# Kernel optimization log

Measured on AMD Instinct MI355X. Metric: run time of the kernel, lower is better.

## Reference

```python
import jax, jax.numpy as jnp
import numpy as np

N = 100_000        # nodes
E = 3_200_000      # edges (avg degree 32)
F_IN = 256         # feature_num
HID = 32           # hard-coded hidden dim in TwoLayerModel
F_OUT = 64         # output_num


def setup_inputs() -> dict:
    key = jax.random.key(0)
    k0, k1, k2, k3 = jax.random.split(key, 4)
    x = jax.random.normal(k0, (N, F_IN), dtype=jnp.float32)
    edge_index = jax.random.randint(k1, (2, E), 0, N, dtype=jnp.int32)
    # glorot-ish init for the two linear weights, zero bias (matches reset_parameters)
    W1 = jax.random.normal(k2, (F_IN, HID), dtype=jnp.float32) * np.float32(1.0 / np.sqrt(F_IN))
    b1 = jnp.zeros((HID,), dtype=jnp.float32)
    W2 = jax.random.normal(k3, (HID, F_OUT), dtype=jnp.float32) * np.float32(1.0 / np.sqrt(HID))
    b2 = jnp.zeros((F_OUT,), dtype=jnp.float32)
    return {"x": x, "edge_index": edge_index, "W1": W1, "b1": b1, "W2": W2, "b2": b2}


def _gcn_propagate(h, row, col, n):
    """Symmetric-normalized sum aggregation: out[i] = sum_{(j->i)} d_j^-1/2 d_i^-1/2 h[j].
    Matches PyG gcn_norm / NewSampleModelLayer edge_weight (deg computed on col)."""
    deg = jax.ops.segment_sum(jnp.ones_like(col, dtype=h.dtype), col, num_segments=n)
    dinv = jnp.where(deg > 0, deg ** -0.5, 0.0)
    norm = dinv[row] * dinv[col]                      # [E']
    return jax.ops.segment_sum(norm[:, None] * h[row], col, num_segments=n)


def reference(x, edge_index, W1, b1, W2, b2):
    n = x.shape[0]
    sl = jnp.arange(n, dtype=edge_index.dtype)
    row = jnp.concatenate([edge_index[0], sl])        # add self-loops
    col = jnp.concatenate([edge_index[1], sl])
    # layer 1: GCNConv(feature_num, 32) -> relu (dropout inactive in eval)
    h = _gcn_propagate(x @ W1, row, col, n) + b1
    h = jax.nn.relu(h)
    # layer 2 (NewSampleModelLayer, eval path): propagate then linear projection
    fr = _gcn_propagate(h, row, col, n)
    return fr @ W2 + b2
```

## Files before the change

kernel.cpp:

```cpp
#include <hip/hip_runtime.h>
#include <hip/hip_fp16.h>
#include <math.h>


#define SHIFT1 8
#define S1 256
#define MAXNB1 400

typedef _Float16 half8 __attribute__((ext_vector_type(8)));
typedef float f32x4 __attribute__((ext_vector_type(4)));

__global__ void k_zero(int* p, int n) {
    int i = blockIdx.x * blockDim.x + threadIdx.x;
    if (i < n) p[i] = 0;
}

__global__ void k_hist1(const int4* __restrict__ cols4, int* __restrict__ bcnt,
                        int e4, int etail, const int* __restrict__ cols, int nb) {
    __shared__ int h[MAXNB1];
    for (int i = threadIdx.x; i < nb; i += blockDim.x) h[i] = 0;
    __syncthreads();
    for (int i = blockIdx.x * blockDim.x + threadIdx.x; i < e4; i += gridDim.x * blockDim.x) {
        int4 c = cols4[i];
        atomicAdd(&h[c.x >> SHIFT1], 1);
        atomicAdd(&h[c.y >> SHIFT1], 1);
        atomicAdd(&h[c.z >> SHIFT1], 1);
        atomicAdd(&h[c.w >> SHIFT1], 1);
    }
    if (blockIdx.x == 0 && threadIdx.x < etail)
        atomicAdd(&h[cols[e4 * 4 + threadIdx.x] >> SHIFT1], 1);
    __syncthreads();
    for (int i = threadIdx.x; i < nb; i += blockDim.x)
        if (h[i]) atomicAdd(&bcnt[i], h[i]);
}

__global__ void k_scan1(const int* __restrict__ bcnt, int* __restrict__ bptr,
                        int* __restrict__ bfill, int nb, int e) {
    __shared__ int sh[512];
    int tid = threadIdx.x;
    int v = (tid < nb) ? bcnt[tid] : 0;
    sh[tid] = v;
    __syncthreads();
    for (int off = 1; off < 512; off <<= 1) {
        int t = (tid >= off) ? sh[tid - off] : 0;
        __syncthreads();
        sh[tid] += t;
        __syncthreads();
    }
    int excl = sh[tid] - v;
    if (tid < nb) { bptr[tid] = excl; bfill[tid] = excl; }
    if (tid == 0) bptr[nb] = e;
}

__launch_bounds__(1024)
__global__ void k_scatter1(const int* __restrict__ rows, const int* __restrict__ cols,
                           int* bfill, unsigned* __restrict__ pk, int e, int nb, int chunk) {
    __shared__ int hist[MAXNB1];
    int tid = threadIdx.x;
    for (int i = tid; i < nb; i += blockDim.x) hist[i] = 0;
    __syncthreads();
    int start = blockIdx.x * chunk;
    int end = min(e, start + chunk);
    for (int i = start + tid; i < end; i += blockDim.x)
        atomicAdd(&hist[cols[i] >> SHIFT1], 1);
    __syncthreads();
    for (int i = tid; i < nb; i += blockDim.x) {
        int c = hist[i];
        if (c) hist[i] = atomicAdd(&bfill[i], c);
    }
    __syncthreads();
    for (int i = start + tid; i < end; i += blockDim.x) {
        int r = rows[i], c = cols[i];
        int pos = atomicAdd(&hist[c >> SHIFT1], 1);
        pk[pos] = ((unsigned)r << SHIFT1) | (unsigned)(c & (S1 - 1));
    }
}

__launch_bounds__(512)
__global__ void k_fine256(const unsigned* __restrict__ pk, const int* __restrict__ bptr,
                          int* __restrict__ erow, int* __restrict__ ptr,
                          float* __restrict__ dinv, int n, int nb) {
    __shared__ int cnt[S1], sh[S1], fill[S1];
    int tid = threadIdx.x, b = blockIdx.x;
    if (tid < S1) cnt[tid] = 0;
    __syncthreads();
    int s = bptr[b], e = bptr[b + 1];
    for (int t = s + tid; t < e; t += 512)
        atomicAdd(&cnt[pk[t] & (S1 - 1)], 1);
    __syncthreads();
    int v = (tid < S1) ? cnt[tid] : 0;
    if (tid < S1) sh[tid] = v;
    __syncthreads();
    for (int off = 1; off < S1; off <<= 1) {
        int t = (tid >= off && tid < S1) ? sh[tid - off] : 0;
        __syncthreads();
        if (tid < S1) sh[tid] += t;
        __syncthreads();
    }
    if (tid < S1) {
        int base = sh[tid] - v;
        fill[tid] = base;
        int node = (b << SHIFT1) + tid;
        if (node < n) {
            ptr[node] = s + base;
            dinv[node] = rsqrtf((float)(v + 1));
        }
    }
    if (b == nb - 1 && tid == 0) ptr[n] = e;
    __syncthreads();
    for (int t = s + tid; t < e; t += 512) {
        unsigned p = pk[t];
        int pos = atomicAdd(&fill[p & (S1 - 1)], 1);
        erow[s + pos] = (int)(p >> SHIFT1);
    }
}

__launch_bounds__(256)
__global__ void k_xw_mfma(const float4* __restrict__ x4, const float4* __restrict__ W1_4,
                          const float* __restrict__ dinv, _Float16* __restrict__ g1h, int n) {
    __shared__ _Float16 xh[64][264];
    __shared__ _Float16 w1t[32][264];
    int tid = threadIdx.x;
    int base = blockIdx.x * 64;
#pragma unroll
    for (int t = 0; t < 16; ++t) {
        int idx = tid + t * 256;
        int row = idx >> 6, c4 = idx & 63;
        float4 v = (base + row < n) ? x4[(size_t)(base + row) * 64 + c4]
                                    : make_float4(0.f, 0.f, 0.f, 0.f);
        __half2 a = __floats2half2_rn(v.x, v.y);
        __half2 b = __floats2half2_rn(v.z, v.w);
        *reinterpret_cast<int2*>(&xh[row][c4 * 4]) = make_int2(*(int*)&a, *(int*)&b);
    }
#pragma unroll
    for (int t = 0; t < 8; ++t) {
        int idx = tid + t * 256;
        int kk = idx >> 3, n4 = idx & 7;
        float4 w = W1_4[idx];
        w1t[n4 * 4 + 0][kk] = (_Float16)w.x;
        w1t[n4 * 4 + 1][kk] = (_Float16)w.y;
        w1t[n4 * 4 + 2][kk] = (_Float16)w.z;
        w1t[n4 * 4 + 3][kk] = (_Float16)w.w;
    }
    __syncthreads();
    int wid = tid >> 6, lane = tid & 63;
    int lrow = lane & 15, kgrp = lane >> 4;
    const _Float16* ap  = &xh[wid * 16 + lrow][kgrp * 8];
    const _Float16* bp0 = &w1t[lrow][kgrp * 8];
    const _Float16* bp1 = &w1t[16 + lrow][kgrp * 8];
    f32x4 acc0 = {0.f, 0.f, 0.f, 0.f}, acc1 = {0.f, 0.f, 0.f, 0.f};
#pragma unroll
    for (int kk = 0; kk < 8; ++kk) {
        half8 a  = *reinterpret_cast<const half8*>(ap + kk * 32);
        half8 b0 = *reinterpret_cast<const half8*>(bp0 + kk * 32);
        half8 b1 = *reinterpret_cast<const half8*>(bp1 + kk * 32);
        acc0 = __builtin_amdgcn_mfma_f32_16x16x32_f16(a, b0, acc0, 0, 0, 0);
        acc1 = __builtin_amdgcn_mfma_f32_16x16x32_f16(a, b1, acc1, 0, 0, 0);
    }
#pragma unroll
    for (int r = 0; r < 4; ++r) {
        int node = base + wid * 16 + kgrp * 4 + r;
        if (node < n) {
            float d = dinv[node];
            g1h[(size_t)node * 32 + lrow]      = (_Float16)(acc0[r] * d);
            g1h[(size_t)node * 32 + 16 + lrow] = (_Float16)(acc1[r] * d);
        }
    }
}

__device__ inline void acc8(float* a, float4 q) {
    const __half2* h = reinterpret_cast<const __half2*>(&q);
#pragma unroll
    for (int i = 0; i < 4; ++i) {
        float2 f = __half22float2(h[i]);
        a[2 * i] += f.x; a[2 * i + 1] += f.y;
    }
}

__launch_bounds__(256)
__global__ void k_agg1(const float4* __restrict__ g1h4, const int* __restrict__ erow,
                       const int* __restrict__ ptr, const float* __restrict__ dinv,
                       const float* __restrict__ b1, int4* __restrict__ g2h4, int n) {
    int tid = threadIdx.x;
    int g = tid >> 2, l = tid & 3;
    int node = blockIdx.x * 64 + g;
    if (node >= n) return;
    int s = ptr[node], e = ptr[node + 1];
    float a[8] = {0, 0, 0, 0, 0, 0, 0, 0};
    float b[8] = {0, 0, 0, 0, 0, 0, 0, 0};
    acc8(a, g1h4[(size_t)node * 4 + l]);
    int t = s;
    for (; t + 7 < e; t += 8) {
        int r0 = erow[t],     r1 = erow[t + 1], r2 = erow[t + 2], r3 = erow[t + 3];
        int r4 = erow[t + 4], r5 = erow[t + 5], r6 = erow[t + 6], r7 = erow[t + 7];
        float4 q0 = g1h4[(size_t)r0 * 4 + l];
        float4 q1 = g1h4[(size_t)r1 * 4 + l];
        float4 q2 = g1h4[(size_t)r2 * 4 + l];
        float4 q3 = g1h4[(size_t)r3 * 4 + l];
        float4 q4 = g1h4[(size_t)r4 * 4 + l];
        float4 q5 = g1h4[(size_t)r5 * 4 + l];
        float4 q6 = g1h4[(size_t)r6 * 4 + l];
        float4 q7 = g1h4[(size_t)r7 * 4 + l];
        acc8(a, q0); acc8(b, q1); acc8(a, q2); acc8(b, q3);
        acc8(a, q4); acc8(b, q5); acc8(a, q6); acc8(b, q7);
    }
    for (; t < e; ++t) acc8(a, g1h4[(size_t)erow[t] * 4 + l]);
    float d = dinv[node];
    float4 bb0 = *reinterpret_cast<const float4*>(&b1[l * 8]);
    float4 bb1 = *reinterpret_cast<const float4*>(&b1[l * 8 + 4]);
    float o[8];
#pragma unroll
    for (int i = 0; i < 8; ++i) {
        float bi = i < 4 ? (&bb0.x)[i] : (&bb1.x)[i - 4];
        float h = fmaf(d, a[i] + b[i], bi);
        o[i] = (h > 0.f ? h : 0.f) * d;
    }
    __half2 h0 = __floats2half2_rn(o[0], o[1]);
    __half2 h1 = __floats2half2_rn(o[2], o[3]);
    __half2 h2 = __floats2half2_rn(o[4], o[5]);
    __half2 h3 = __floats2half2_rn(o[6], o[7]);
    g2h4[(size_t)node * 4 + l] = make_int4(*(int*)&h0, *(int*)&h1, *(int*)&h2, *(int*)&h3);
}

__launch_bounds__(256)
__global__ void k_agg2(const float4* __restrict__ g2h4, const int* __restrict__ erow,
                       const int* __restrict__ ptr, const float* __restrict__ dinv,
                       const float* __restrict__ W2, const float* __restrict__ b2,
                       float* __restrict__ out, int n) {
    __shared__ _Float16 frh[64][40];
    __shared__ _Float16 w2h[64][40];
    int tid = threadIdx.x;
    {
        int c = tid >> 2, kb = (tid & 3) * 8;
#pragma unroll
        for (int i = 0; i < 8; ++i)
            w2h[c][kb + i] = (_Float16)W2[(kb + i) * 64 + c];
    }
    int g = tid >> 2, l = tid & 3;
    int node = blockIdx.x * 64 + g;
    float a[8] = {0, 0, 0, 0, 0, 0, 0, 0};
    float b[8] = {0, 0, 0, 0, 0, 0, 0, 0};
    float d = 0.f;
    if (node < n) {
        int s = ptr[node], e = ptr[node + 1];
        acc8(a, g2h4[(size_t)node * 4 + l]);
        int t = s;
        for (; t + 7 < e; t += 8) {
            int r0 = erow[t],     r1 = erow[t + 1], r2 = erow[t + 2], r3 = erow[t + 3];
            int r4 = erow[t + 4], r5 = erow[t + 5], r6 = erow[t + 6], r7 = erow[t + 7];
            float4 q0 = g2h4[(size_t)r0 * 4 + l];
            float4 q1 = g2h4[(size_t)r1 * 4 + l];
            float4 q2 = g2h4[(size_t)r2 * 4 + l];
            float4 q3 = g2h4[(size_t)r3 * 4 + l];
            float4 q4 = g2h4[(size_t)r4 * 4 + l];
            float4 q5 = g2h4[(size_t)r5 * 4 + l];
            float4 q6 = g2h4[(size_t)r6 * 4 + l];
            float4 q7 = g2h4[(size_t)r7 * 4 + l];
            acc8(a, q0); acc8(b, q1); acc8(a, q2); acc8(b, q3);
            acc8(a, q4); acc8(b, q5); acc8(a, q6); acc8(b, q7);
        }
        for (; t < e; ++t) acc8(a, g2h4[(size_t)erow[t] * 4 + l]);
        d = dinv[node];
    }
    {
        _Float16 tmp[8];
#pragma unroll
        for (int i = 0; i < 8; ++i) tmp[i] = (_Float16)(d * (a[i] + b[i]));
        *reinterpret_cast<half8*>(&frh[g][l * 8]) = *reinterpret_cast<half8*>(tmp);
    }
    __syncthreads();
    int w = tid >> 6, lane = tid & 63;
    int lcol = lane & 15, kgrp = lane >> 4;
    half8 afrag = *reinterpret_cast<const half8*>(&frh[w * 16 + lcol][kgrp * 8]);
    half8 bf0 = *reinterpret_cast<const half8*>(&w2h[lcol][kgrp * 8]);
    half8 bf1 = *reinterpret_cast<const half8*>(&w2h[16 + lcol][kgrp * 8]);
    half8 bf2 = *reinterpret_cast<const half8*>(&w2h[32 + lcol][kgrp * 8]);
    half8 bf3 = *reinterpret_cast<const half8*>(&w2h[48 + lcol][kgrp * 8]);
    f32x4 c0 = {0.f, 0.f, 0.f, 0.f}, c1 = c0, c2 = c0, c3 = c0;
    c0 = __builtin_amdgcn_mfma_f32_16x16x32_f16(afrag, bf0, c0, 0, 0, 0);
    c1 = __builtin_amdgcn_mfma_f32_16x16x32_f16(afrag, bf1, c1, 0, 0, 0);
    c2 = __builtin_amdgcn_mfma_f32_16x16x32_f16(afrag, bf2, c2, 0, 0, 0);
    c3 = __builtin_amdgcn_mfma_f32_16x16x32_f16(afrag, bf3, c3, 0, 0, 0);
    float bi0 = b2[lcol], bi1 = b2[16 + lcol], bi2 = b2[32 + lcol], bi3 = b2[48 + lcol];
#pragma unroll
    for (int r = 0; r < 4; ++r) {
        int node2 = blockIdx.x * 64 + w * 16 + kgrp * 4 + r;
        if (node2 < n) {
            float* op = &out[(size_t)node2 * 64];
            op[lcol]      = c0[r] + bi0;
            op[16 + lcol] = c1[r] + bi1;
            op[32 + lcol] = c2[r] + bi2;
            op[48 + lcol] = c3[r] + bi3;
        }
    }
}

extern "C" void kernel_launch(void* const* d_in, const int* in_sizes, int n_in,
                              void* d_out, int out_size, void* d_ws, size_t ws_size,
                              hipStream_t stream) {
    const float* x  = (const float*)d_in[0];
    const int*   ei = (const int*)d_in[1];
    const float* W1 = (const float*)d_in[2];
    const float* b1 = (const float*)d_in[3];
    const float* W2 = (const float*)d_in[4];
    const float* b2 = (const float*)d_in[5];
    float* out = (float*)d_out;

    const int N = in_sizes[0] / 256;
    const int E = in_sizes[1] / 2;
    const int* rows = ei;
    const int* cols = ei + E;
    const int NB1 = (N + S1 - 1) >> SHIFT1;

    size_t sz0 = (size_t)E > (size_t)N * 16 ? (size_t)E : (size_t)N * 16;
    unsigned* pk  = (unsigned*)d_ws;
    _Float16* g1h = (_Float16*)d_ws;
    int*      erow = (int*)((char*)d_ws + sz0 * 4);
    _Float16* g2h  = (_Float16*)(erow + E);
    float*    dinv = (float*)((char*)(erow + E) + (size_t)N * 32 * 2);
    int*      ptr  = (int*)(dinv + N);
    int*      bptr1 = ptr + (N + 1);
    int*      bcnt1 = bptr1 + (NB1 + 1);
    int*      bfill1 = bcnt1 + NB1;

    const int B = 256;
    const int e4 = E / 4, etail = E - e4 * 4;
    const int SCB = 256;
    const int chunk = (E + SCB - 1) / SCB;
    const int nblk64 = (N + 63) / 64;

    k_zero<<<(NB1 + B - 1) / B, B, 0, stream>>>(bcnt1, NB1);
    k_hist1<<<256, B, 0, stream>>>((const int4*)cols, bcnt1, e4, etail, cols, NB1);
    k_scan1<<<1, 512, 0, stream>>>(bcnt1, bptr1, bfill1, NB1, E);
    k_scatter1<<<SCB, 1024, 0, stream>>>(rows, cols, bfill1, pk, E, NB1, chunk);
    k_fine256<<<NB1, 512, 0, stream>>>(pk, bptr1, erow, ptr, dinv, N, NB1);
    k_xw_mfma<<<nblk64, B, 0, stream>>>((const float4*)x, (const float4*)W1, dinv, g1h, N);
    k_agg1<<<nblk64, B, 0, stream>>>((const float4*)g1h, erow, ptr, dinv, b1, (int4*)g2h, N);
    k_agg2<<<nblk64, B, 0, stream>>>((const float4*)g2h, erow, ptr, dinv, W2, b2, out, N);
}
```

Before: 187.8 us.

## Pad CSR neighbor lists to multiples of 8 and share indices via wave shuffles

```diff
diff --git a/kernel.cpp b/kernel.cpp
--- a/kernel.cpp
+++ b/kernel.cpp
@@ -6,6 +6,7 @@
 #define SHIFT1 8
 #define S1 256
 #define MAXNB1 400
+#define BSLACK 2048
 
 typedef _Float16 half8 __attribute__((ext_vector_type(8)));
 typedef float f32x4 __attribute__((ext_vector_type(4)));
@@ -13,6 +14,12 @@
 __global__ void k_zero(int* p, int n) {
     int i = blockIdx.x * blockDim.x + threadIdx.x;
     if (i < n) p[i] = 0;
+}
+
+__global__ void k_zrow(_Float16* g1h, _Float16* g2h, int n) {
+    int i = threadIdx.x;
+    if (i < 16)      ((int*)(g1h + (size_t)n * 32))[i] = 0;
+    else if (i < 32) ((int*)(g2h + (size_t)n * 32))[i - 16] = 0;
 }
 
 __global__ void k_hist1(const int4* __restrict__ cols4, int* __restrict__ bcnt,
@@ -78,9 +85,9 @@
 
 __launch_bounds__(512)
 __global__ void k_fine256(const unsigned* __restrict__ pk, const int* __restrict__ bptr,
-                          int* __restrict__ erow, int* __restrict__ ptr,
+                          int* __restrict__ erow, int2* __restrict__ ptr2,
                           float* __restrict__ dinv, int n, int nb) {
-    __shared__ int cnt[S1], sh[S1], fill[S1];
+    __shared__ int cnt[S1], sh[S1], fill[S1], pvs[S1];
     int tid = threadIdx.x, b = blockIdx.x;
     if (tid < S1) cnt[tid] = 0;
     __syncthreads();
@@ -88,8 +95,13 @@
     for (int t = s + tid; t < e; t += 512)
         atomicAdd(&cnt[pk[t] & (S1 - 1)], 1);
     __syncthreads();
-    int v = (tid < S1) ? cnt[tid] : 0;
-    if (tid < S1) sh[tid] = v;
+    int v = 0, pv = 0;
+    if (tid < S1) {
+        v = cnt[tid];
+        pv = (v + 7) & ~7;
+        sh[tid] = pv;
+        pvs[tid] = pv;
+    }
     __syncthreads();
     for (int off = 1; off < S1; off <<= 1) {
         int t = (tid >= off && tid < S1) ? sh[tid - off] : 0;
@@ -97,21 +109,29 @@
         if (tid < S1) sh[tid] += t;
         __syncthreads();
     }
+    int mybase = 0;
     if (tid < S1) {
-        int base = sh[tid] - v;
-        fill[tid] = base;
+        int base = sh[tid] - pv;
+        int ebase = ((s + b * BSLACK) + 7) & ~7;
+        mybase = ebase + base;
+        fill[tid] = mybase;
         int node = (b << SHIFT1) + tid;
         if (node < n) {
-            ptr[node] = s + base;
+            ptr2[node] = make_int2(mybase, mybase + pv);
             dinv[node] = rsqrtf((float)(v + 1));
         }
     }
-    if (b == nb - 1 && tid == 0) ptr[n] = e;
     __syncthreads();
     for (int t = s + tid; t < e; t += 512) {
         unsigned p = pk[t];
         int pos = atomicAdd(&fill[p & (S1 - 1)], 1);
-        erow[s + pos] = (int)(p >> SHIFT1);
+        erow[pos] = (int)(p >> SHIFT1);
+    }
+    __syncthreads();
+    if (tid < S1) {
+        int endv = mybase + v;
+        int endp = mybase + pvs[tid];
+        for (int i = endv; i < endp; ++i) erow[i] = n;
     }
 }
 
@@ -177,34 +197,44 @@
     }
 }
 
+#define GATHER_BODY(gsrc)                                                         \
+    if (s < e) {                                                                  \
+        int lb = (tid & 63) & 60;                                                 \
+        int2 pr = *reinterpret_cast<const int2*>(&erow[s + 2 * l]);               \
+        for (int t = s; t < e; t += 8) {                                          \
+            int2 prn = *reinterpret_cast<const int2*>(&erow[t + 8 + 2 * l]);      \
+            int r0 = __shfl(pr.x, lb + 0, 64), r1 = __shfl(pr.y, lb + 0, 64);     \
+            int r2 = __shfl(pr.x, lb + 1, 64), r3 = __shfl(pr.y, lb + 1, 64);     \
+            int r4 = __shfl(pr.x, lb + 2, 64), r5 = __shfl(pr.y, lb + 2, 64);     \
+            int r6 = __shfl(pr.x, lb + 3, 64), r7 = __shfl(pr.y, lb + 3, 64);     \
+            float4 q0 = gsrc[(size_t)r0 * 4 + l];                                 \
+            float4 q1 = gsrc[(size_t)r1 * 4 + l];                                 \
+            float4 q2 = gsrc[(size_t)r2 * 4 + l];                                 \
+            float4 q3 = gsrc[(size_t)r3 * 4 + l];                                 \
+            float4 q4 = gsrc[(size_t)r4 * 4 + l];                                 \
+            float4 q5 = gsrc[(size_t)r5 * 4 + l];                                 \
+            float4 q6 = gsrc[(size_t)r6 * 4 + l];                                 \
+            float4 q7 = gsrc[(size_t)r7 * 4 + l];                                 \
+            acc8(a, q0); acc8(b, q1); acc8(a, q2); acc8(b, q3);                   \
+            acc8(a, q4); acc8(b, q5); acc8(a, q6); acc8(b, q7);                   \
+            pr = prn;                                                             \
+        }                                                                         \
+    }
+
 __launch_bounds__(256)
 __global__ void k_agg1(const float4* __restrict__ g1h4, const int* __restrict__ erow,
-                       const int* __restrict__ ptr, const float* __restrict__ dinv,
+                       const int2* __restrict__ ptr2, const float* __restrict__ dinv,
                        const float* __restrict__ b1, int4* __restrict__ g2h4, int n) {
     int tid = threadIdx.x;
     int g = tid >> 2, l = tid & 3;
     int node = blockIdx.x * 64 + g;
     if (node >= n) return;
-    int s = ptr[node], e = ptr[node + 1];
+    int2 pe = ptr2[node];
+    int s = pe.x, e = pe.y;
     float a[8] = {0, 0, 0, 0, 0, 0, 0, 0};
     float b[8] = {0, 0, 0, 0, 0, 0, 0, 0};
     acc8(a, g1h4[(size_t)node * 4 + l]);
-    int t = s;
-    for (; t + 7 < e; t += 8) {
-        int r0 = erow[t],     r1 = erow[t + 1], r2 = erow[t + 2], r3 = erow[t + 3];
-        int r4 = erow[t + 4], r5 = erow[t + 5], r6 = erow[t + 6], r7 = erow[t + 7];
-        float4 q0 = g1h4[(size_t)r0 * 4 + l];
-        float4 q1 = g1h4[(size_t)r1 * 4 + l];
-        float4 q2 = g1h4[(size_t)r2 * 4 + l];
-        float4 q3 = g1h4[(size_t)r3 * 4 + l];
-        float4 q4 = g1h4[(size_t)r4 * 4 + l];
-        float4 q5 = g1h4[(size_t)r5 * 4 + l];
-        float4 q6 = g1h4[(size_t)r6 * 4 + l];
-        float4 q7 = g1h4[(size_t)r7 * 4 + l];
-        acc8(a, q0); acc8(b, q1); acc8(a, q2); acc8(b, q3);
-        acc8(a, q4); acc8(b, q5); acc8(a, q6); acc8(b, q7);
-    }
-    for (; t < e; ++t) acc8(a, g1h4[(size_t)erow[t] * 4 + l]);
+    GATHER_BODY(g1h4)
     float d = dinv[node];
     float4 bb0 = *reinterpret_cast<const float4*>(&b1[l * 8]);
     float4 bb1 = *reinterpret_cast<const float4*>(&b1[l * 8 + 4]);
@@ -224,7 +254,7 @@
 
 __launch_bounds__(256)
 __global__ void k_agg2(const float4* __restrict__ g2h4, const int* __restrict__ erow,
-                       const int* __restrict__ ptr, const float* __restrict__ dinv,
+                       const int2* __restrict__ ptr2, const float* __restrict__ dinv,
                        const float* __restrict__ W2, const float* __restrict__ b2,
                        float* __restrict__ out, int n) {
     __shared__ _Float16 frh[64][40];
@@ -242,24 +272,10 @@
     float b[8] = {0, 0, 0, 0, 0, 0, 0, 0};
     float d = 0.f;
     if (node < n) {
-        int s = ptr[node], e = ptr[node + 1];
+        int2 pe = ptr2[node];
+        int s = pe.x, e = pe.y;
         acc8(a, g2h4[(size_t)node * 4 + l]);
-        int t = s;
-        for (; t + 7 < e; t += 8) {
-            int r0 = erow[t],     r1 = erow[t + 1], r2 = erow[t + 2], r3 = erow[t + 3];
-            int r4 = erow[t + 4], r5 = erow[t + 5], r6 = erow[t + 6], r7 = erow[t + 7];
-            float4 q0 = g2h4[(size_t)r0 * 4 + l];
-            float4 q1 = g2h4[(size_t)r1 * 4 + l];
-            float4 q2 = g2h4[(size_t)r2 * 4 + l];
-            float4 q3 = g2h4[(size_t)r3 * 4 + l];
-            float4 q4 = g2h4[(size_t)r4 * 4 + l];
-            float4 q5 = g2h4[(size_t)r5 * 4 + l];
-            float4 q6 = g2h4[(size_t)r6 * 4 + l];
-            float4 q7 = g2h4[(size_t)r7 * 4 + l];
-            acc8(a, q0); acc8(b, q1); acc8(a, q2); acc8(b, q3);
-            acc8(a, q4); acc8(b, q5); acc8(a, q6); acc8(b, q7);
-        }
-        for (; t < e; ++t) acc8(a, g2h4[(size_t)erow[t] * 4 + l]);
+        GATHER_BODY(g2h4)
         d = dinv[node];
     }
     {
@@ -312,14 +328,16 @@
     const int* cols = ei + E;
     const int NB1 = (N + S1 - 1) >> SHIFT1;
 
-    size_t sz0 = (size_t)E > (size_t)N * 16 ? (size_t)E : (size_t)N * 16;
-    unsigned* pk  = (unsigned*)d_ws;
-    _Float16* g1h = (_Float16*)d_ws;
-    int*      erow = (int*)((char*)d_ws + sz0 * 4);
-    _Float16* g2h  = (_Float16*)(erow + E);
-    float*    dinv = (float*)((char*)(erow + E) + (size_t)N * 32 * 2);
-    int*      ptr  = (int*)(dinv + N);
-    int*      bptr1 = ptr + (N + 1);
+    size_t g1w = (size_t)(N + 1) * 16;
+    size_t sz0 = (size_t)E > g1w ? (size_t)E : g1w;
+    size_t szE = (size_t)E + (size_t)NB1 * BSLACK + 64;
+    unsigned* pk   = (unsigned*)d_ws;
+    _Float16* g1h  = (_Float16*)d_ws;
+    int*      erow = (int*)d_ws + sz0;
+    _Float16* g2h  = (_Float16*)(erow + szE);
+    float*    dinv = (float*)((int*)(erow + szE) + g1w);
+    int2*     ptr2 = (int2*)(dinv + N);
+    int*      bptr1 = (int*)(ptr2 + N);
     int*      bcnt1 = bptr1 + (NB1 + 1);
     int*      bfill1 = bcnt1 + NB1;
 
@@ -333,8 +351,9 @@
     k_hist1<<<256, B, 0, stream>>>((const int4*)cols, bcnt1, e4, etail, cols, NB1);
     k_scan1<<<1, 512, 0, stream>>>(bcnt1, bptr1, bfill1, NB1, E);
     k_scatter1<<<SCB, 1024, 0, stream>>>(rows, cols, bfill1, pk, E, NB1, chunk);
-    k_fine256<<<NB1, 512, 0, stream>>>(pk, bptr1, erow, ptr, dinv, N, NB1);
+    k_fine256<<<NB1, 512, 0, stream>>>(pk, bptr1, erow, ptr2, dinv, N, NB1);
+    k_zrow<<<1, 64, 0, stream>>>(g1h, g2h, N);
     k_xw_mfma<<<nblk64, B, 0, stream>>>((const float4*)x, (const float4*)W1, dinv, g1h, N);
-    k_agg1<<<nblk64, B, 0, stream>>>((const float4*)g1h, erow, ptr, dinv, b1, (int4*)g2h, N);
-    k_agg2<<<nblk64, B, 0, stream>>>((const float4*)g2h, erow, ptr, dinv, W2, b2, out, N);
-}
+    k_agg1<<<nblk64, B, 0, stream>>>((const float4*)g1h, erow, ptr2, dinv, b1, (int4*)g2h, N);
+    k_agg2<<<nblk64, B, 0, stream>>>((const float4*)g2h, erow, ptr2, dinv, W2, b2, out, N);
+}
```

Result: no change. 187.1 us (median of 2 runs) (-0.4%).
